# Optimization experiments

Hardware: AMD Instinct MI355X
Metric: run time of the kernel (lower is better)

The kernel has to match this reference:

```python
import jax, jax.numpy as jnp
import numpy as np

B, S, D = 2, 2048, 1024
H = 16
HD = D // H  # head_dim = 64
NEG = -1e30  # finite stand-in for -inf; masked entries are zeroed after softmax so math matches


def setup_inputs() -> dict:
    key = jax.random.key(0)
    ks = jax.random.split(key, 10)
    q = jax.random.normal(ks[0], (B, S, D), dtype=jnp.float32)
    k = jax.random.normal(ks[1], (B, S, D), dtype=jnp.float32)
    v = jax.random.normal(ks[2], (B, S, D), dtype=jnp.float32)
    mask = jax.random.randint(ks[3], (B, S), 0, 2).astype(bool)
    s = 1.0 / np.sqrt(D)
    Wq = jax.random.uniform(ks[4], (D, D), jnp.float32, -s, s)
    bq = jax.random.uniform(ks[5], (D,), jnp.float32, -s, s)
    Wk = jax.random.uniform(ks[6], (D, D), jnp.float32, -s, s)
    bk = jax.random.uniform(ks[7], (D,), jnp.float32, -s, s)
    Wv = jax.random.uniform(ks[8], (D, D), jnp.float32, -s, s)
    bv = jax.random.uniform(ks[9], (D,), jnp.float32, -s, s)
    return {"q": q, "k": k, "v": v, "mask": mask,
            "Wq": Wq, "bq": bq, "Wk": Wk, "bk": bk, "Wv": Wv, "bv": bv}


def _split_heads(x):
    # [B,S,D] -> [H,B,S,HD]  (matches permute(2,0,1,3) in torch)
    return x.reshape(B, S, H, HD).transpose(2, 0, 1, 3)


def reference(q, k, v, mask, Wq, bq, Wk, bk, Wv, bv):
    mq = _split_heads(q @ Wq.T + bq)
    mk = _split_heads(k @ Wk.T + bk)
    mv = _split_heads(v @ Wv.T + bv)
    # scores: [H,B,Sq,Sk]
    scores = jnp.einsum('hbqd,hbkd->hbqk', mq, mk) / jnp.sqrt(jnp.float32(HD))
    pair_mask = (mask[:, :, None] & mask[:, None, :])[None]  # [1,B,S,S]
    scores = jnp.where(pair_mask, scores, NEG)
    attn = jax.nn.softmax(scores, axis=-1)
    attn = jnp.where(pair_mask, attn, 0.0)
    out = jnp.einsum('hbqk,hbkd->hbqd', attn, mv)
    # [H,B,S,HD] -> [B,S,D]
    return out.transpose(1, 2, 0, 3).reshape(B, S, H * HD)
```

## Files before the change

kernel.cpp:

```cpp
#include <hip/hip_runtime.h>
#include <math.h>

#define B_ 2
#define S_ 2048
#define D_ 1024
#define H_ 16
#define HD_ 64
#define LOG2E 1.44269504088896340736f

typedef __bf16 bf16_t;
typedef bf16_t bf16x8 __attribute__((ext_vector_type(8)));
typedef bf16_t bf16x4v __attribute__((ext_vector_type(4)));
typedef float f32x4 __attribute__((ext_vector_type(4)));

#define GLOBAL_LOAD_LDS16(gp, lp)                                              \
    __builtin_amdgcn_global_load_lds(                                          \
        (const __attribute__((address_space(1))) void*)(gp),                   \
        (__attribute__((address_space(3))) void*)(lp), 16, 0, 0)

static __device__ __forceinline__ float exp2_raw(float x)
{
    float r;
    asm("v_exp_f32 %0, %1" : "=v"(r) : "v"(x));
    return r;
}

__global__ __launch_bounds__(256) void cvt_kernel(
    const float* __restrict__ q, const float* __restrict__ k,
    const float* __restrict__ v, const float* __restrict__ wq,
    const float* __restrict__ wk, const float* __restrict__ wv,
    bf16_t* __restrict__ qb, bf16_t* __restrict__ kb, bf16_t* __restrict__ vb,
    bf16_t* __restrict__ wqb, bf16_t* __restrict__ wkb, bf16_t* __restrict__ wvb)
{
    const size_t NT = (size_t)1 << 20;
    const size_t NW = (size_t)1 << 18;
    size_t g = (size_t)blockIdx.x * 256 + threadIdx.x;

    const float* src;
    bf16_t* dst;
    size_t off;
    if (g < 3 * NT) {
        int t = (int)(g >> 20);
        off = (g & (NT - 1)) * 4;
        src = (t == 0) ? q : (t == 1) ? k : v;
        dst = (t == 0) ? qb : (t == 1) ? kb : vb;
    } else {
        size_t gw = g - 3 * NT;
        if (gw >= 3 * NW) return;
        int t = (int)(gw >> 18);
        off = (gw & (NW - 1)) * 4;
        src = (t == 0) ? wq : (t == 1) ? wk : wv;
        dst = (t == 0) ? wqb : (t == 1) ? wkb : wvb;
    }

    float4 f = *(const float4*)(src + off);
    bf16x4v o;
    o[0] = (bf16_t)f.x; o[1] = (bf16_t)f.y;
    o[2] = (bf16_t)f.z; o[3] = (bf16_t)f.w;
    *(bf16x4v*)(dst + off) = o;
}

__global__ __launch_bounds__(256) void proj_mfma(
    const bf16_t* __restrict__ X0, const bf16_t* __restrict__ X1,
    const bf16_t* __restrict__ X2, const bf16_t* __restrict__ W0,
    const bf16_t* __restrict__ W1, const bf16_t* __restrict__ W2,
    const float* __restrict__ b0, const float* __restrict__ b1,
    const float* __restrict__ b2, bf16_t* __restrict__ o0,
    bf16_t* __restrict__ o1, bf16_t* __restrict__ o2)
{
    __shared__ __align__(16) bf16_t As[128 * 32];
    __shared__ __align__(16) bf16_t Bs[128 * 32];

    const int z = blockIdx.z;
    const bf16_t* X = (z == 0) ? X0 : (z == 1) ? X1 : X2;
    const bf16_t* W = (z == 0) ? W0 : (z == 1) ? W1 : W2;
    const float* bias = (z == 0) ? b0 : (z == 1) ? b1 : b2;
    bf16_t* out = (z == 0) ? o0 : (z == 1) ? o1 : o2;
    const float oscale = (z == 0) ? (0.125f * LOG2E) : 1.0f;

    const int tid  = threadIdx.x;
    const int w    = tid >> 6;
    const int lane = tid & 63;
    const int L    = lane & 15;
    const int quad = lane >> 4;
    const int wr   = (w >> 1) * 64;
    const int wc   = (w & 1) * 64;
    const int row0 = blockIdx.x * 128;
    const int col0 = blockIdx.y * 128;

    const int lr = lane >> 2;
    const int lc = (lane & 3) * 8;

    f32x4 acc[4][4];
    #pragma unroll
    for (int i = 0; i < 4; ++i)
        #pragma unroll
        for (int j = 0; j < 4; ++j) {
            acc[i][j][0] = 0.f; acc[i][j][1] = 0.f;
            acc[i][j][2] = 0.f; acc[i][j][3] = 0.f;
        }

    for (int k0 = 0; k0 < D_; k0 += 32) {
        __syncthreads();
        #pragma unroll
        for (int i = 0; i < 2; ++i) {
            const int rA = i * 64 + w * 16;
            GLOBAL_LOAD_LDS16(X + (size_t)(row0 + rA + lr) * D_ + k0 + lc,
                              &As[rA * 32]);
            GLOBAL_LOAD_LDS16(W + (size_t)(col0 + rA + lr) * D_ + k0 + lc,
                              &Bs[rA * 32]);
        }
        __syncthreads();

        bf16x8 aF[4], bF[4];
        #pragma unroll
        for (int t = 0; t < 4; ++t) {
            aF[t] = *(const bf16x8*)&As[(wr + t * 16 + L) * 32 + quad * 8];
            bF[t] = *(const bf16x8*)&Bs[(wc + t * 16 + L) * 32 + quad * 8];
        }
        #pragma unroll
        for (int mt = 0; mt < 4; ++mt)
            #pragma unroll
            for (int nt = 0; nt < 4; ++nt)
                acc[mt][nt] = __builtin_amdgcn_mfma_f32_16x16x32_bf16(
                    aF[mt], bF[nt], acc[mt][nt], 0, 0, 0);
    }

    if (z == 2) {
        #pragma unroll
        for (int nt = 0; nt < 4; ++nt) {
            const int j  = col0 + wc + nt * 16 + L;
            const float bval = bias[j];
            const int h  = j >> 6;
            const int hd = j & 63;
            #pragma unroll
            for (int mt = 0; mt < 4; ++mt) {
                const int n0 = row0 + wr + mt * 16 + quad * 4;
                const int b  = n0 >> 11;
                const int s  = n0 & (S_ - 1);
                bf16x4v p;
                #pragma unroll
                for (int r = 0; r < 4; ++r)
                    p[r] = (bf16_t)(acc[mt][nt][r] + bval);
                *(bf16x4v*)(out + ((size_t)(b * H_ + h) * HD_ + hd) * S_ + s) = p;
            }
        }
    } else {
        #pragma unroll
        for (int nt = 0; nt < 4; ++nt) {
            const int j  = col0 + wc + nt * 16 + L;
            const float bval = bias[j];
            const int h  = j >> 6;
            const int hd = j & 63;
            #pragma unroll
            for (int mt = 0; mt < 4; ++mt)
                #pragma unroll
                for (int r = 0; r < 4; ++r) {
                    const int n = row0 + wr + mt * 16 + quad * 4 + r;
                    const int b = n >> 11;
                    const int s = n & (S_ - 1);
                    out[((((size_t)b * H_ + h) * S_ + s) * HD_) + hd] =
                        (bf16_t)((acc[mt][nt][r] + bval) * oscale);
                }
        }
    }
}

__global__ __launch_bounds__(256) void attn_kernel(
    const bf16_t* __restrict__ Q, const bf16_t* __restrict__ K,
    const bf16_t* __restrict__ Vt, const int* __restrict__ mask,
    float* __restrict__ out)
{
    __shared__ bf16_t Ks[2][64 * 64];
    __shared__ bf16_t Vs[2][64 * 64];
    __shared__ bf16_t Pt[4][32 * 64];

    const int tid  = threadIdx.x;
    const int w    = tid >> 6;
    const int lane = tid & 63;
    const int L    = lane & 15;
    const int quad = lane >> 4;
    const int L7   = L & 7;

    const float VB = -8.0f * LOG2E;
    const float MB = -1.44269504e30f;

    const int orig = blockIdx.x + 16 * (blockIdx.y + 16 * blockIdx.z);
    const int work = (orig & 7) * 64 + (orig >> 3);
    const int q0   = (work & 15) * 128;
    const int h    = (work >> 4) & 15;
    const int b    = work >> 8;
    const int bh   = b * H_ + h;

    const bf16_t* kbase = K  + (size_t)bh * S_ * HD_;
    const bf16_t* vbase = Vt + (size_t)bh * HD_ * S_;
    const int*    mrow  = mask + b * S_;

    const int sr  = tid >> 3;
    const int c8  = tid & 7;
    const int sc2 = c8 * 8;
    const int swz = ((c8 ^ (sr & 7)) * 8);
    const int st0 = sr * 64 + swz;
    const int st1 = (sr + 32) * 64 + swz;

    bf16x8 aQ[2][2];
    #pragma unroll
    for (int qb = 0; qb < 2; ++qb) {
        const bf16_t* qp = Q + ((size_t)bh * S_ + q0 + w * 32 + qb * 16 + L) * HD_;
        aQ[qb][0] = *(const bf16x8*)(qp + quad * 8);
        aQ[qb][1] = *(const bf16x8*)(qp + 32 + quad * 8);
    }

    f32x4 o[2][4];
    #pragma unroll
    for (int qb = 0; qb < 2; ++qb)
        #pragma unroll
        for (int f = 0; f < 4; ++f) {
            o[qb][f][0]=0.f; o[qb][f][1]=0.f; o[qb][f][2]=0.f; o[qb][f][3]=0.f;
        }
    f32x4 ol[2];
    #pragma unroll
    for (int qb = 0; qb < 2; ++qb) {
        ol[qb][0]=0.f; ol[qb][1]=0.f; ol[qb][2]=0.f; ol[qb][3]=0.f;
    }

    bf16x8 ones;
    #pragma unroll
    for (int i = 0; i < 8; ++i) ones[i] = (bf16_t)1.0f;

    bf16x8 kr0, kr1, vr0, vr1;
    f32x4  bias_c[4], bias_n[4];
    kr0 = *(const bf16x8*)(kbase + (size_t)sr * HD_ + sc2);
    kr1 = *(const bf16x8*)(kbase + (size_t)(sr + 32) * HD_ + sc2);
    vr0 = *(const bf16x8*)(vbase + (size_t)sr * S_ + sc2);
    vr1 = *(const bf16x8*)(vbase + (size_t)(sr + 32) * S_ + sc2);
    #pragma unroll
    for (int f = 0; f < 4; ++f) {
        int4 mi = *(const int4*)(mrow + f * 16 + quad * 4);
        bias_c[f][0] = mi.x ? VB : MB;
        bias_c[f][1] = mi.y ? VB : MB;
        bias_c[f][2] = mi.z ? VB : MB;
        bias_c[f][3] = mi.w ? VB : MB;
    }

    *(bf16x8*)&Ks[0][st0] = kr0;
    *(bf16x8*)&Ks[0][st1] = kr1;
    *(bf16x8*)&Vs[0][st0] = vr0;
    *(bf16x8*)&Vs[0][st1] = vr1;

    kr0 = *(const bf16x8*)(kbase + (size_t)(64 + sr) * HD_ + sc2);
    kr1 = *(const bf16x8*)(kbase + (size_t)(64 + sr + 32) * HD_ + sc2);
    vr0 = *(const bf16x8*)(vbase + (size_t)sr * S_ + 64 + sc2);
    vr1 = *(const bf16x8*)(vbase + (size_t)(sr + 32) * S_ + 64 + sc2);
    #pragma unroll
    for (int f = 0; f < 4; ++f) {
        int4 mi = *(const int4*)(mrow + 64 + f * 16 + quad * 4);
        bias_n[f][0] = mi.x ? VB : MB;
        bias_n[f][1] = mi.y ? VB : MB;
        bias_n[f][2] = mi.z ? VB : MB;
        bias_n[f][3] = mi.w ? VB : MB;
    }

    __syncthreads();

    for (int t = 0; t < 32; ++t) {
        const int cur = t & 1;
        bf16_t* ks  = &Ks[cur][0];
        bf16_t* vs  = &Vs[cur][0];

        if (t < 31) {
            bf16_t* ksn = &Ks[cur ^ 1][0];
            bf16_t* vsn = &Vs[cur ^ 1][0];
            *(bf16x8*)&ksn[st0] = kr0;
            *(bf16x8*)&ksn[st1] = kr1;
            *(bf16x8*)&vsn[st0] = vr0;
            *(bf16x8*)&vsn[st1] = vr1;
        }
        if (t < 30) {
            const int kn = (t + 2) * 64;
            kr0 = *(const bf16x8*)(kbase + (size_t)(kn + sr) * HD_ + sc2);
            kr1 = *(const bf16x8*)(kbase + (size_t)(kn + sr + 32) * HD_ + sc2);
            vr0 = *(const bf16x8*)(vbase + (size_t)sr * S_ + kn + sc2);
            vr1 = *(const bf16x8*)(vbase + (size_t)(sr + 32) * S_ + kn + sc2);
        }

        bf16x8 aK[4][2];
        #pragma unroll
        for (int f = 0; f < 4; ++f) {
            const int row = (f * 16 + L) * 64;
            aK[f][0] = *(const bf16x8*)&ks[row + ((quad ^ L7) * 8)];
            aK[f][1] = *(const bf16x8*)&ks[row + (((4 | quad) ^ L7) * 8)];
        }

        bf16_t* pw = &Pt[w][0];
        #pragma unroll
        for (int qb = 0; qb < 2; ++qb) {
            const int prow = (qb * 16 + L) * 64;
            #pragma unroll
            for (int f = 0; f < 4; ++f) {
                f32x4 z = bias_c[f];
                z = __builtin_amdgcn_mfma_f32_16x16x32_bf16(aK[f][0], aQ[qb][0], z, 0, 0, 0);
                z = __builtin_amdgcn_mfma_f32_16x16x32_bf16(aK[f][1], aQ[qb][1], z, 0, 0, 0);
                bf16x4v p4;
                p4[0] = (bf16_t)exp2_raw(z[0]);
                p4[1] = (bf16_t)exp2_raw(z[1]);
                p4[2] = (bf16_t)exp2_raw(z[2]);
                p4[3] = (bf16_t)exp2_raw(z[3]);
                *(bf16x4v*)&pw[prow + (((f * 2 + (quad >> 1)) ^ L7) * 8) + (quad & 1) * 4] = p4;
            }
        }

        #pragma unroll
        for (int f = 0; f < 4; ++f) bias_c[f] = bias_n[f];
        if (t < 30) {
            const int kn = (t + 2) * 64;
            #pragma unroll
            for (int f = 0; f < 4; ++f) {
                int4 mi = *(const int4*)(mrow + kn + f * 16 + quad * 4);
                bias_n[f][0] = mi.x ? VB : MB;
                bias_n[f][1] = mi.y ? VB : MB;
                bias_n[f][2] = mi.z ? VB : MB;
                bias_n[f][3] = mi.w ? VB : MB;
            }
        }

        bf16x8 aP[2][2];
        #pragma unroll
        for (int qb = 0; qb < 2; ++qb) {
            const int prow = (qb * 16 + L) * 64;
            aP[qb][0] = *(const bf16x8*)&pw[prow + ((quad ^ L7) * 8)];
            aP[qb][1] = *(const bf16x8*)&pw[prow + (((4 | quad) ^ L7) * 8)];
            ol[qb] = __builtin_amdgcn_mfma_f32_16x16x32_bf16(aP[qb][0], ones, ol[qb], 0, 0, 0);
            ol[qb] = __builtin_amdgcn_mfma_f32_16x16x32_bf16(aP[qb][1], ones, ol[qb], 0, 0, 0);
        }

        #pragma unroll
        for (int f = 0; f < 4; ++f) {
            const int row = (f * 16 + L) * 64;
            bf16x8 bV0 = *(const bf16x8*)&vs[row + ((quad ^ L7) * 8)];
            bf16x8 bV1 = *(const bf16x8*)&vs[row + (((4 | quad) ^ L7) * 8)];
            #pragma unroll
            for (int qb = 0; qb < 2; ++qb) {
                o[qb][f] = __builtin_amdgcn_mfma_f32_16x16x32_bf16(aP[qb][0], bV0, o[qb][f], 0, 0, 0);
                o[qb][f] = __builtin_amdgcn_mfma_f32_16x16x32_bf16(aP[qb][1], bV1, o[qb][f], 0, 0, 0);
            }
        }

        __syncthreads();
    }

    #pragma unroll
    for (int qb = 0; qb < 2; ++qb) {
        const int4 m4 = *(const int4*)&mrow[q0 + w * 32 + qb * 16 + quad * 4];
        float inv[4];
        inv[0] = (m4.x && ol[qb][0] > 0.f) ? (1.0f / ol[qb][0]) : 0.0f;
        inv[1] = (m4.y && ol[qb][1] > 0.f) ? (1.0f / ol[qb][1]) : 0.0f;
        inv[2] = (m4.z && ol[qb][2] > 0.f) ? (1.0f / ol[qb][2]) : 0.0f;
        inv[3] = (m4.w && ol[qb][3] > 0.f) ? (1.0f / ol[qb][3]) : 0.0f;

        float* obase = out + ((size_t)b * S_ + q0 + w * 32 + qb * 16 + quad * 4) * D_ + h * HD_;
        #pragma unroll
        for (int f = 0; f < 4; ++f)
            #pragma unroll
            for (int r = 0; r < 4; ++r)
                obase[r * D_ + f * 16 + L] = o[qb][f][r] * inv[r];
    }
}

extern "C" void kernel_launch(void* const* d_in, const int* in_sizes, int n_in,
                              void* d_out, int out_size, void* d_ws, size_t ws_size,
                              hipStream_t stream)
{
    const float* q    = (const float*)d_in[0];
    const float* k    = (const float*)d_in[1];
    const float* v    = (const float*)d_in[2];
    const int*   mask = (const int*)d_in[3];
    const float* Wq   = (const float*)d_in[4];
    const float* bq   = (const float*)d_in[5];
    const float* Wk   = (const float*)d_in[6];
    const float* bk   = (const float*)d_in[7];
    const float* Wv   = (const float*)d_in[8];
    const float* bv   = (const float*)d_in[9];
    float* out = (float*)d_out;

    const size_t PE = (size_t)B_ * S_ * D_;
    const size_t WE = (size_t)D_ * D_;

    bf16_t* qb  = (bf16_t*)d_ws;
    bf16_t* kb  = qb + PE;
    bf16_t* vb  = kb + PE;
    bf16_t* wqb = vb + PE;
    bf16_t* wkb = wqb + WE;
    bf16_t* wvb = wkb + WE;
    bf16_t* mq  = wvb + WE;
    bf16_t* mk  = mq + PE;
    bf16_t* vt  = mk + PE;

    const size_t ngroups = 3 * (PE / 4) + 3 * (WE / 4);
    dim3 cgrid((ngroups + 255) / 256);
    cvt_kernel<<<cgrid, 256, 0, stream>>>(q, k, v, Wq, Wk, Wv,
                                          qb, kb, vb, wqb, wkb, wvb);

    dim3 pgrid(4096 / 128, 1024 / 128, 3);
    proj_mfma<<<pgrid, 256, 0, stream>>>(qb, kb, vb, wqb, wkb, wvb,
                                         bq, bk, bv, mq, mk, vt);

    dim3 agrid(S_ / 128, H_, B_);
    attn_kernel<<<agrid, 256, 0, stream>>>(mq, mk, vt, mask, out);
}
```

Before: 218.2 us.

## Split attention over two key halves and merge partials in a combine kernel

Each (batch, head, query-tile) attention block now handles only half of the key sequence, which doubles the attention grid to give more blocks per CU and a shorter per-block loop. Unnormalized partial outputs and row sums go to `out` and to a scratch buffer that reuses the already-consumed bf16 input region of the workspace. A new elementwise kernel adds the two partials, applies the mask and reciprocal normalization, and writes the final output. This works because softmax uses a fixed bias rather than a running max, so partial sums add directly. The cost is an extra kernel launch and several tens of MB of extra global memory traffic for the partials.

Result: slower. 228.2 us (+4.6%).

```diff
diff --git a/kernel.cpp b/kernel.cpp
--- a/kernel.cpp
+++ b/kernel.cpp
@@ -169,7 +169,7 @@
 __global__ __launch_bounds__(256) void attn_kernel(
     const bf16_t* __restrict__ Q, const bf16_t* __restrict__ K,
     const bf16_t* __restrict__ Vt, const int* __restrict__ mask,
-    float* __restrict__ out)
+    float* __restrict__ out, float* __restrict__ po, float* __restrict__ pl)
 {
     __shared__ bf16_t Ks[2][64 * 64];
     __shared__ bf16_t Vs[2][64 * 64];
@@ -186,15 +186,17 @@
     const float MB = -1.44269504e30f;
 
     const int orig = blockIdx.x + 16 * (blockIdx.y + 16 * blockIdx.z);
-    const int work = (orig & 7) * 64 + (orig >> 3);
+    const int work = (orig & 7) * 128 + (orig >> 3);
     const int q0   = (work & 15) * 128;
     const int h    = (work >> 4) & 15;
-    const int b    = work >> 8;
+    const int bhf  = work >> 8;
+    const int b    = bhf >> 1;
+    const int half = bhf & 1;
     const int bh   = b * H_ + h;
 
-    const bf16_t* kbase = K  + (size_t)bh * S_ * HD_;
-    const bf16_t* vbase = Vt + (size_t)bh * HD_ * S_;
-    const int*    mrow  = mask + b * S_;
+    const bf16_t* kbase = K  + ((size_t)bh * S_ + half * 1024) * HD_;
+    const bf16_t* vbase = Vt + (size_t)bh * HD_ * S_ + half * 1024;
+    const int*    mrow  = mask + b * S_ + half * 1024;
 
     const int sr  = tid >> 3;
     const int c8  = tid & 7;
@@ -263,12 +265,12 @@
 
     __syncthreads();
 
-    for (int t = 0; t < 32; ++t) {
+    for (int t = 0; t < 16; ++t) {
         const int cur = t & 1;
         bf16_t* ks  = &Ks[cur][0];
         bf16_t* vs  = &Vs[cur][0];
 
-        if (t < 31) {
+        if (t < 15) {
             bf16_t* ksn = &Ks[cur ^ 1][0];
             bf16_t* vsn = &Vs[cur ^ 1][0];
             *(bf16x8*)&ksn[st0] = kr0;
@@ -276,7 +278,7 @@
             *(bf16x8*)&vsn[st0] = vr0;
             *(bf16x8*)&vsn[st1] = vr1;
         }
-        if (t < 30) {
+        if (t < 14) {
             const int kn = (t + 2) * 64;
             kr0 = *(const bf16x8*)(kbase + (size_t)(kn + sr) * HD_ + sc2);
             kr1 = *(const bf16x8*)(kbase + (size_t)(kn + sr + 32) * HD_ + sc2);
@@ -312,7 +314,7 @@
 
         #pragma unroll
         for (int f = 0; f < 4; ++f) bias_c[f] = bias_n[f];
-        if (t < 30) {
+        if (t < 14) {
             const int kn = (t + 2) * 64;
             #pragma unroll
             for (int f = 0; f < 4; ++f) {
@@ -349,22 +351,48 @@
         __syncthreads();
     }
 
+    float* dst = half ? po : out;
     #pragma unroll
     for (int qb = 0; qb < 2; ++qb) {
-        const int4 m4 = *(const int4*)&mrow[q0 + w * 32 + qb * 16 + quad * 4];
-        float inv[4];
-        inv[0] = (m4.x && ol[qb][0] > 0.f) ? (1.0f / ol[qb][0]) : 0.0f;
-        inv[1] = (m4.y && ol[qb][1] > 0.f) ? (1.0f / ol[qb][1]) : 0.0f;
-        inv[2] = (m4.z && ol[qb][2] > 0.f) ? (1.0f / ol[qb][2]) : 0.0f;
-        inv[3] = (m4.w && ol[qb][3] > 0.f) ? (1.0f / ol[qb][3]) : 0.0f;
-
-        float* obase = out + ((size_t)b * S_ + q0 + w * 32 + qb * 16 + quad * 4) * D_ + h * HD_;
+        float* obase = dst + ((size_t)b * S_ + q0 + w * 32 + qb * 16 + quad * 4) * D_ + h * HD_;
         #pragma unroll
         for (int f = 0; f < 4; ++f)
             #pragma unroll
             for (int r = 0; r < 4; ++r)
-                obase[r * D_ + f * 16 + L] = o[qb][f][r] * inv[r];
-    }
+                obase[r * D_ + f * 16 + L] = o[qb][f][r];
+
+        if (L == 0) {
+            float* plh = pl + (size_t)half * (B_ * H_ * S_)
+                            + (size_t)bh * S_ + q0 + w * 32 + qb * 16 + quad * 4;
+            #pragma unroll
+            for (int r = 0; r < 4; ++r)
+                plh[r] = ol[qb][r];
+        }
+    }
+}
+
+__global__ __launch_bounds__(256) void combine_kernel(
+    const float* __restrict__ po, const float* __restrict__ pl,
+    const int* __restrict__ mask, float* __restrict__ out)
+{
+    size_t e = ((size_t)blockIdx.x * 256 + threadIdx.x) * 4;
+    const int d = (int)(e & (D_ - 1));
+    const int s = (int)((e >> 10) & (S_ - 1));
+    const int b = (int)(e >> 21);
+    const int h = d >> 6;
+
+    const size_t li = (size_t)(b * H_ + h) * S_ + s;
+    float l = pl[li] + pl[(size_t)B_ * H_ * S_ + li];
+    float inv = (mask[b * S_ + s] && l > 0.f) ? (1.0f / l) : 0.0f;
+
+    float4 a = *(const float4*)(out + e);
+    float4 c = *(const float4*)(po + e);
+    float4 r;
+    r.x = (a.x + c.x) * inv;
+    r.y = (a.y + c.y) * inv;
+    r.z = (a.z + c.z) * inv;
+    r.w = (a.w + c.w) * inv;
+    *(float4*)(out + e) = r;
 }
 
 extern "C" void kernel_launch(void* const* d_in, const int* in_sizes, int n_in,
@@ -396,6 +424,9 @@
     bf16_t* mk  = mq + PE;
     bf16_t* vt  = mk + PE;
 
+    float* po = (float*)d_ws;
+    float* pl = (float*)d_ws + PE;
+
     const size_t ngroups = 3 * (PE / 4) + 3 * (WE / 4);
     dim3 cgrid((ngroups + 255) / 256);
     cvt_kernel<<<cgrid, 256, 0, stream>>>(q, k, v, Wq, Wk, Wv,
@@ -405,6 +436,9 @@
     proj_mfma<<<pgrid, 256, 0, stream>>>(qb, kb, vb, wqb, wkb, wvb,
                                          bq, bk, bv, mq, mk, vt);
 
-    dim3 agrid(S_ / 128, H_, B_);
-    attn_kernel<<<agrid, 256, 0, stream>>>(mq, mk, vt, mask, out);
-}
+    dim3 agrid(S_ / 128, H_, B_ * 2);
+    attn_kernel<<<agrid, 256, 0, stream>>>(mq, mk, vt, mask, out, po, pl);
+
+    dim3 ggrid((unsigned)(PE / 4 / 256));
+    combine_kernel<<<ggrid, 256, 0, stream>>>(po, pl, mask, out);
+}
```
